# Kernel tuning notes

Hardware: AMD Instinct MI355X
Metric: run time of the kernel (lower is better)

Reference implementation:

```python
import jax, jax.numpy as jnp
import numpy as np

B, S, D_IN, D_OUT = 4, 2048, 1024, 1024

def setup_inputs() -> dict:
    key = jax.random.key(0)
    k1, k2, k3, k4 = jax.random.split(key, 4)
    sc = 0.02
    return {
        "x": jax.random.normal(k1, (B, S, D_IN), dtype=jnp.float32),
        "Wq": jax.random.normal(k2, (D_OUT, D_IN), dtype=jnp.float32) * sc,
        "Wk": jax.random.normal(k3, (D_OUT, D_IN), dtype=jnp.float32) * sc,
        "Wv": jax.random.normal(k4, (D_OUT, D_IN), dtype=jnp.float32) * sc,
    }

def reference(x, Wq, Wk, Wv):
    # torch Linear: y = x @ W.T  (weights stored [out, in])
    b, n, _ = x.shape
    q = jnp.einsum('bnd,od->bno', x, Wq)  # [B,S,D_OUT]
    k = jnp.einsum('bnd,od->bno', x, Wk)
    v = jnp.einsum('bnd,od->bno', x, Wv)
    scores = jnp.einsum('bqd,bkd->bqk', q, k)  # [B,S,S]
    # causal mask: positions j > i masked to -inf BEFORE scaling (matches source)
    causal = jnp.triu(jnp.ones((n, n), dtype=bool), k=1)
    scores = jnp.where(causal[None, :, :], -jnp.inf, scores)
    scale = 1.0 / jnp.sqrt(jnp.float32(k.shape[-1]))
    attn = jax.nn.softmax(scores * scale, axis=-1)
    # NOTE: source calls dropout but discards its output -> no-op
    return jnp.einsum('bqk,bkd->bqd', attn, v)
```

## Files before the change

kernel.cpp:

```cpp
#include <hip/hip_runtime.h>
#include <hip/hip_bf16.h>
#include <hip/hip_fp16.h>


using bf16 = __hip_bfloat16;
typedef __bf16 bf16x8 __attribute__((ext_vector_type(8)));
typedef float f32x4 __attribute__((ext_vector_type(4)));

__device__ __forceinline__ void load_lds_16B(const void* g, void* l) {
  __builtin_amdgcn_global_load_lds(
      (const __attribute__((address_space(1))) unsigned int*)g,
      (__attribute__((address_space(3))) unsigned int*)l, 16, 0, 0);
}

template <int N>
__device__ __forceinline__ void waitcnt_vm() {
  if constexpr (N == 6) asm volatile("s_waitcnt vmcnt(6)" ::: "memory");
  else if constexpr (N == 5) asm volatile("s_waitcnt vmcnt(5)" ::: "memory");
  else asm volatile("s_waitcnt vmcnt(0)" ::: "memory");
}

__device__ __forceinline__ int swz(int o) { return o ^ (((o >> 7) & 7) << 4); }

template <int M_REP, int OUT, bool CSKIP, bool KLIM>
__global__ __launch_bounds__(512, 2) void gemm8p(
    const bf16* __restrict__ A, const bf16* __restrict__ Bm, void* __restrict__ Cv,
    int K, int lda, int ldb, int ldc, long sAz, long sBz, long sCzBytes) {
  constexpr int BM = M_REP * 32, BN = 256;
  constexpr int MH2 = M_REP / 2;
  constexpr int AKC = BM * 64;
  constexpr int BKC = BN * 64;
  constexpr int DBSTR = 2 * AKC + 2 * BKC;
  constexpr int ACALLS = AKC / 8192;
  constexpr int VM_LEAVE = ACALLS + 4;

  const int tn = blockIdx.x, tm = blockIdx.y, z = blockIdx.z;
  if (CSKIP && tn > tm) return;
  A += (long)z * sAz;
  Bm += (long)z * sBz;
  char* C = (char*)Cv + (long)z * sCzBytes;

  int kEnd = K;
  if (KLIM) kEnd = min(tm * BM + BM, K);
  const int nt = kEnd >> 6;
  const int NI = nt >> 1;

  __shared__ __align__(128) char sm[2 * DBSTR];
  const int tid = threadIdx.x, lane = tid & 63, wv = tid >> 6;
  const int wr = wv >> 2, wc = wv & 3;
  const int ldsw = wv * 1024;

  const char* srcA[ACALLS];
  const char* srcB[2];
#pragma unroll
  for (int c = 0; c < ACALLS; c++) {
    int os = swz(c * 8192 + tid * 16);
    srcA[c] = (const char*)(A + ((long)tm * BM + (os >> 6)) * lda) + (os & 63);
  }
#pragma unroll
  for (int c = 0; c < 2; c++) {
    int os = swz(c * 8192 + tid * 16);
    srcB[c] = (const char*)(Bm + ((long)tn * BN + (os >> 6)) * ldb) + (os & 63);
  }
  auto stageA = [&](int t, int kc) {
#pragma unroll
    for (int c = 0; c < ACALLS; c++)
      load_lds_16B(srcA[c] + (long)t * 128 + kc * 64,
                   sm + (t & 1) * DBSTR + kc * AKC + c * 8192 + ldsw);
  };
  auto stageB = [&](int t, int kc) {
#pragma unroll
    for (int c = 0; c < 2; c++)
      load_lds_16B(srcB[c] + (long)t * 128 + kc * 64,
                   sm + (t & 1) * DBSTR + 2 * AKC + kc * BKC + c * 8192 + ldsw);
  };

  int aoff[M_REP], boff[4];
#pragma unroll
  for (int m = 0; m < M_REP; m++)
    aoff[m] = swz((wr * (M_REP * 16) + m * 16 + (lane & 15)) * 64 + (lane >> 4) * 16);
#pragma unroll
  for (int n = 0; n < 4; n++)
    boff[n] = 2 * AKC + swz((wc * 64 + n * 16 + (lane & 15)) * 64 + (lane >> 4) * 16);

  f32x4 acc[M_REP][4] = {};
  bf16x8 bfr[2][4];
  bf16x8 afrA[MH2], afrB[MH2];

#define LDB(DBUF, KC)                                                          \
  _Pragma("unroll") for (int n = 0; n < 4; n++)                                \
      bfr[KC][n] = *(const bf16x8*)(sm + (DBUF)*DBSTR + (KC)*BKC + boff[n]);
#define LDA(DBUF, KC, MH, DST)                                                 \
  _Pragma("unroll") for (int m = 0; m < MH2; m++)                              \
      DST[m] = *(const bf16x8*)(sm + (DBUF)*DBSTR + (KC)*AKC + aoff[(MH)*MH2 + m]);
#define MFMAS(KC, MH, AFR)                                                     \
  __builtin_amdgcn_s_setprio(1);                                               \
  _Pragma("unroll") for (int m = 0; m < MH2; m++)                              \
      _Pragma("unroll") for (int n = 0; n < 4; n++)                            \
          acc[(MH)*MH2 + m][n] = __builtin_amdgcn_mfma_f32_16x16x32_bf16(      \
              AFR[m], bfr[KC][n], acc[(MH)*MH2 + m][n], 0, 0, 0);              \
  __builtin_amdgcn_s_setprio(0);
#define BAR1()                                                                 \
  __builtin_amdgcn_s_barrier();                                                \
  asm volatile("s_waitcnt lgkmcnt(0)" ::: "memory");                           \
  __builtin_amdgcn_sched_barrier(0);
#define BAR2() __builtin_amdgcn_s_barrier();

  stageB(0, 0); stageA(0, 0); stageB(0, 1); stageA(0, 1);
  stageB(1, 0); stageA(1, 0); stageB(1, 1);
  waitcnt_vm<VM_LEAVE>();
  __builtin_amdgcn_s_barrier();

  for (int i = 0; i < NI - 1; i++) {
    const int ta = 2 * i, tb = 2 * i + 1;
    LDB(0, 0); LDA(0, 0, 0, afrA); stageA(tb, 1);     BAR1(); MFMAS(0, 0, afrA); BAR2();
    LDA(0, 0, 1, afrB);            stageB(ta + 2, 0); BAR1(); MFMAS(0, 1, afrB); BAR2();
    LDB(0, 1); LDA(0, 1, 0, afrA); stageA(ta + 2, 0); BAR1(); MFMAS(1, 0, afrA); BAR2();
    LDA(0, 1, 1, afrB);            stageB(ta + 2, 1);
    waitcnt_vm<VM_LEAVE>();                           BAR1(); MFMAS(1, 1, afrB); BAR2();
    LDB(1, 0); LDA(1, 0, 0, afrA); stageA(ta + 2, 1); BAR1(); MFMAS(0, 0, afrA); BAR2();
    LDA(1, 0, 1, afrB);            stageB(tb + 2, 0); BAR1(); MFMAS(0, 1, afrB); BAR2();
    LDB(1, 1); LDA(1, 1, 0, afrA); stageA(tb + 2, 0); BAR1(); MFMAS(1, 0, afrA); BAR2();
    LDA(1, 1, 1, afrB);            stageB(tb + 2, 1);
    waitcnt_vm<VM_LEAVE>();                           BAR1(); MFMAS(1, 1, afrB); BAR2();
  }
  {
    const int tb = nt - 1;
    LDB(0, 0); LDA(0, 0, 0, afrA); stageA(tb, 1); BAR1(); MFMAS(0, 0, afrA); BAR2();
    LDA(0, 0, 1, afrB);                           BAR1(); MFMAS(0, 1, afrB); BAR2();
    LDB(0, 1); LDA(0, 1, 0, afrA);                BAR1(); MFMAS(1, 0, afrA); BAR2();
    LDA(0, 1, 1, afrB); waitcnt_vm<0>();          BAR1(); MFMAS(1, 1, afrB); BAR2();
    LDB(1, 0); LDA(1, 0, 0, afrA);                BAR1(); MFMAS(0, 0, afrA); BAR2();
    LDA(1, 0, 1, afrB);                           BAR1(); MFMAS(0, 1, afrB); BAR2();
    LDB(1, 1); LDA(1, 1, 0, afrA);                BAR1(); MFMAS(1, 0, afrA); BAR2();
    LDA(1, 1, 1, afrB);                           BAR1(); MFMAS(1, 1, afrB); BAR2();
  }
#undef LDB
#undef LDA
#undef MFMAS
#undef BAR1
#undef BAR2

  const int cr0 = tm * BM + wr * (M_REP * 16) + (lane >> 4) * 4;
  const int cc0 = tn * BN + wc * 64 + (lane & 15);
#pragma unroll
  for (int m = 0; m < M_REP; m++)
#pragma unroll
    for (int n = 0; n < 4; n++)
#pragma unroll
      for (int j = 0; j < 4; j++) {
        long row = cr0 + m * 16 + j;
        long col = cc0 + n * 16;
        if (OUT == 1)
          ((bf16*)C)[row * (long)ldc + col] = __float2bfloat16(acc[m][n][j]);
        else if (OUT == 2)
          ((__half*)C)[row * (long)ldc + col] = __float2half(acc[m][n][j]);
        else
          ((float*)C)[row * (long)ldc + col] = acc[m][n][j];
      }
}

__global__ __launch_bounds__(256) void cvt_all(const float* __restrict__ x,
                                               const float* __restrict__ wq,
                                               const float* __restrict__ wk,
                                               const float* __restrict__ wv,
                                               bf16* __restrict__ xb,
                                               bf16* __restrict__ wb) {
  const int b = blockIdx.x;
  const float* src;
  bf16* dst;
  int i;
  if (b < 8192) { src = x; dst = xb; i = b * 256 + threadIdx.x; }
  else if (b < 9216) { src = wq; dst = wb; i = (b - 8192) * 256 + threadIdx.x; }
  else if (b < 10240) { src = wk; dst = wb + 1048576; i = (b - 9216) * 256 + threadIdx.x; }
  else { src = wv; dst = wb + 2097152; i = (b - 10240) * 256 + threadIdx.x; }
  float4 f = ((const float4*)src)[i];
  union { bf16 h[4]; uint2 u; } o;
  o.h[0] = __float2bfloat16(f.x);
  o.h[1] = __float2bfloat16(f.y);
  o.h[2] = __float2bfloat16(f.z);
  o.h[3] = __float2bfloat16(f.w);
  ((uint2*)dst)[i] = o.u;
}

typedef short short4v __attribute__((ext_vector_type(4)));

__global__ __launch_bounds__(256) void softmax_causal(const __half* __restrict__ Sc,
                                                      bf16* __restrict__ P) {
  const int i = blockIdx.x, b = blockIdx.y;
  const long base = ((long)b * 2048 + i) * 2048;
  const __half* row = Sc + base;
  bf16* prow = P + base;
  const int tid = threadIdx.x, lane = tid & 63, wv = tid >> 6;
  const int len = i + 1;

  float v[8];
  float m = -3.3e38f;
  {
    const int j0 = tid * 8;
    union { short4v s[2]; __half h[8]; } u;
    u.s[0] = *(const short4v*)(row + j0);
    u.s[1] = *(const short4v*)(row + j0 + 4);
#pragma unroll
    for (int e = 0; e < 8; e++) {
      float t = __half2float(u.h[e]);
      v[e] = (j0 + e < len) ? t : -3.3e38f;
      m = fmaxf(m, v[e]);
    }
  }
  for (int o = 32; o; o >>= 1) m = fmaxf(m, __shfl_xor(m, o));
  __shared__ float redm[4], reds[4];
  if (lane == 0) redm[wv] = m;
  __syncthreads();
  m = fmaxf(fmaxf(redm[0], redm[1]), fmaxf(redm[2], redm[3]));

  const float scale = 0.03125f;
  float e8[8];
  float s = 0.f;
  {
    const int j0 = tid * 8;
#pragma unroll
    for (int e = 0; e < 8; e++) {
      float t = (j0 + e < len) ? __expf((v[e] - m) * scale) : 0.f;
      e8[e] = t;
      s += t;
    }
  }
  for (int o = 32; o; o >>= 1) s += __shfl_xor(s, o);
  if (lane == 0) reds[wv] = s;
  __syncthreads();
  s = reds[0] + reds[1] + reds[2] + reds[3];
  const float inv = 1.0f / s;
  {
    const int j0 = tid * 8;
    union { bf16 h[8]; uint4 u4; } o;
#pragma unroll
    for (int e = 0; e < 8; e++) o.h[e] = __float2bfloat16(e8[e] * inv);
    *(uint4*)(prow + j0) = o.u4;
  }
}

__global__ __launch_bounds__(256) void transposeV(const bf16* __restrict__ V,
                                                  bf16* __restrict__ Vt) {
  __shared__ bf16 t[32][33];
  const int b = blockIdx.z;
  const int s0 = blockIdx.x << 5;
  const int d0 = blockIdx.y << 5;
  const bf16* Vb = V + (long)b * 2048 * 3072;
  bf16* Vtb = Vt + (long)b * 1024 * 2048;
  const int lx = threadIdx.x & 31, ly = threadIdx.x >> 5;
#pragma unroll
  for (int r = 0; r < 32; r += 8)
    t[r + ly][lx] = Vb[(long)(s0 + r + ly) * 3072 + d0 + lx];
  __syncthreads();
#pragma unroll
  for (int r = 0; r < 32; r += 8)
    Vtb[(long)(d0 + r + ly) * 2048 + s0 + lx] = t[lx][r + ly];
}

extern "C" void kernel_launch(void* const* d_in, const int* in_sizes, int n_in,
                              void* d_out, int out_size, void* d_ws, size_t ws_size,
                              hipStream_t stream) {
  const float* x = (const float*)d_in[0];
  const float* Wq = (const float*)d_in[1];
  const float* Wk = (const float*)d_in[2];
  const float* Wv = (const float*)d_in[3];

  const long MBy = 1 << 20;
  char* ws = (char*)d_ws;
  bf16* Cqkv = (bf16*)(ws);
  bf16* Vt = (bf16*)(ws + 48 * MBy);
  bf16* P = (bf16*)(ws + 64 * MBy);
  __half* Sc = (__half*)(ws + 96 * MBy);
  bf16* xb = (bf16*)(ws + 96 * MBy);
  bf16* Wb = (bf16*)(ws + 112 * MBy);

  cvt_all<<<11264, 256, 0, stream>>>(x, Wq, Wk, Wv, xb, Wb);

  gemm8p<4, 1, false, false><<<dim3(12, 64), 512, 0, stream>>>(
      xb, Wb, Cqkv, 1024, 1024, 1024, 3072, 0L, 0L, 0L);

  transposeV<<<dim3(64, 32, 4), 256, 0, stream>>>(Cqkv + 2048, Vt);

  gemm8p<8, 2, true, false><<<dim3(8, 8, 4), 512, 0, stream>>>(
      Cqkv, Cqkv + 1024, Sc, 1024, 3072, 3072, 2048,
      2048L * 3072, 2048L * 3072, 2048L * 2048 * 2);

  softmax_causal<<<dim3(2048, 4), 256, 0, stream>>>(Sc, P);

  gemm8p<4, 0, false, true><<<dim3(4, 16, 4), 512, 0, stream>>>(
      P, Vt, d_out, 2048, 2048, 2048, 1024,
      2048L * 2048, 1024L * 2048, 2048L * 1024 * 4);
}
```

Before: 169.4 us.

## Generalize GEMM kernel tiling and retune tiles per stage with reversed causal order

Replaces the fixed 512-thread GEMM template with one parameterized by block tile, warp grid, staging thread count and occupancy. Each of the three GEMMs (QKV projection, QK^T scores, PV) gets its own tile shape and warp count. Finer-grained causal block skipping on the score GEMM, plus reversed row order for the K-limited PV GEMM so the heaviest tiles launch first. This trades register and LDS pressure and occupancy for better load balance and reuse, and relies on the padded even tile count staying correct for the causal PV K-range.

```diff
diff --git a/kernel.cpp b/kernel.cpp
--- a/kernel.cpp
+++ b/kernel.cpp
@@ -15,80 +15,92 @@
 
 template <int N>
 __device__ __forceinline__ void waitcnt_vm() {
-  if constexpr (N == 6) asm volatile("s_waitcnt vmcnt(6)" ::: "memory");
+  if constexpr (N == 10) asm volatile("s_waitcnt vmcnt(10)" ::: "memory");
+  else if constexpr (N == 9) asm volatile("s_waitcnt vmcnt(9)" ::: "memory");
+  else if constexpr (N == 8) asm volatile("s_waitcnt vmcnt(8)" ::: "memory");
+  else if constexpr (N == 6) asm volatile("s_waitcnt vmcnt(6)" ::: "memory");
   else if constexpr (N == 5) asm volatile("s_waitcnt vmcnt(5)" ::: "memory");
   else asm volatile("s_waitcnt vmcnt(0)" ::: "memory");
 }
 
 __device__ __forceinline__ int swz(int o) { return o ^ (((o >> 7) & 7) << 4); }
 
-template <int M_REP, int OUT, bool CSKIP, bool KLIM>
-__global__ __launch_bounds__(512, 2) void gemm8p(
+template <int BM, int BN, int WM, int WN, int STHR, int OCC, int OUT,
+          bool CSKIP, bool KLIM>
+__global__ __launch_bounds__(WM* WN * 64, OCC) void gemmT(
     const bf16* __restrict__ A, const bf16* __restrict__ Bm, void* __restrict__ Cv,
     int K, int lda, int ldb, int ldc, long sAz, long sBz, long sCzBytes) {
-  constexpr int BM = M_REP * 32, BN = 256;
-  constexpr int MH2 = M_REP / 2;
+  constexpr int MR = BM / WM / 16, NR = BN / WN / 16, MH2 = MR / 2;
   constexpr int AKC = BM * 64;
   constexpr int BKC = BN * 64;
-  constexpr int DBSTR = 2 * AKC + 2 * BKC;
-  constexpr int ACALLS = AKC / 8192;
-  constexpr int VM_LEAVE = ACALLS + 4;
-
-  const int tn = blockIdx.x, tm = blockIdx.y, z = blockIdx.z;
-  if (CSKIP && tn > tm) return;
+  constexpr int DBSTR = 2 * (AKC + BKC);
+  constexpr int CHUNK = STHR * 16;
+  constexpr int ACALLS = AKC / CHUNK;
+  constexpr int BCALLS = BKC / CHUNK;
+  constexpr int VM_LEAVE = ACALLS + 2 * BCALLS;
+
+  const int tn = blockIdx.x, z = blockIdx.z;
+  const int tm = KLIM ? (gridDim.y - 1 - blockIdx.y) : blockIdx.y;
+  if (CSKIP && (long)tn * BN >= (long)tm * BM + BM) return;
   A += (long)z * sAz;
   Bm += (long)z * sBz;
   char* C = (char*)Cv + (long)z * sCzBytes;
 
   int kEnd = K;
   if (KLIM) kEnd = min(tm * BM + BM, K);
-  const int nt = kEnd >> 6;
+  int nt = kEnd >> 6;
+  if (KLIM) nt = (nt + 1) & ~1;
   const int NI = nt >> 1;
 
   __shared__ __align__(128) char sm[2 * DBSTR];
   const int tid = threadIdx.x, lane = tid & 63, wv = tid >> 6;
-  const int wr = wv >> 2, wc = wv & 3;
-  const int ldsw = wv * 1024;
-
+  const int wr = wv / WN, wc = wv % WN;
+  const int ldsw = (tid >> 6) * 1024;
+
+  const int ts = (tid < STHR) ? tid : 0;
   const char* srcA[ACALLS];
-  const char* srcB[2];
+  const char* srcB[BCALLS];
 #pragma unroll
   for (int c = 0; c < ACALLS; c++) {
-    int os = swz(c * 8192 + tid * 16);
+    int os = swz(c * CHUNK + ts * 16);
     srcA[c] = (const char*)(A + ((long)tm * BM + (os >> 6)) * lda) + (os & 63);
   }
 #pragma unroll
-  for (int c = 0; c < 2; c++) {
-    int os = swz(c * 8192 + tid * 16);
+  for (int c = 0; c < BCALLS; c++) {
+    int os = swz(c * CHUNK + ts * 16);
     srcB[c] = (const char*)(Bm + ((long)tn * BN + (os >> 6)) * ldb) + (os & 63);
   }
   auto stageA = [&](int t, int kc) {
-#pragma unroll
-    for (int c = 0; c < ACALLS; c++)
-      load_lds_16B(srcA[c] + (long)t * 128 + kc * 64,
-                   sm + (t & 1) * DBSTR + kc * AKC + c * 8192 + ldsw);
+    if (tid < STHR) {
+#pragma unroll
+      for (int c = 0; c < ACALLS; c++)
+        load_lds_16B(srcA[c] + (long)t * 128 + kc * 64,
+                     sm + (t & 1) * DBSTR + kc * AKC + c * CHUNK + ldsw);
+    }
   };
   auto stageB = [&](int t, int kc) {
-#pragma unroll
-    for (int c = 0; c < 2; c++)
-      load_lds_16B(srcB[c] + (long)t * 128 + kc * 64,
-                   sm + (t & 1) * DBSTR + 2 * AKC + kc * BKC + c * 8192 + ldsw);
+    if (tid < STHR) {
+#pragma unroll
+      for (int c = 0; c < BCALLS; c++)
+        load_lds_16B(srcB[c] + (long)t * 128 + kc * 64,
+                     sm + (t & 1) * DBSTR + 2 * AKC + kc * BKC + c * CHUNK + ldsw);
+    }
   };
 
-  int aoff[M_REP], boff[4];
-#pragma unroll
-  for (int m = 0; m < M_REP; m++)
-    aoff[m] = swz((wr * (M_REP * 16) + m * 16 + (lane & 15)) * 64 + (lane >> 4) * 16);
-#pragma unroll
-  for (int n = 0; n < 4; n++)
-    boff[n] = 2 * AKC + swz((wc * 64 + n * 16 + (lane & 15)) * 64 + (lane >> 4) * 16);
-
-  f32x4 acc[M_REP][4] = {};
-  bf16x8 bfr[2][4];
+  int aoff[MR], boff[NR];
+#pragma unroll
+  for (int m = 0; m < MR; m++)
+    aoff[m] = swz((wr * (BM / WM) + m * 16 + (lane & 15)) * 64 + (lane >> 4) * 16);
+#pragma unroll
+  for (int n = 0; n < NR; n++)
+    boff[n] = 2 * AKC + swz((wc * (BN / WN) + n * 16 + (lane & 15)) * 64 + (lane >> 4) * 16);
+
+  f32x4 acc[MR][NR] = {};
+  bf16x8 bfr[2][NR];
   bf16x8 afrA[MH2], afrB[MH2];
 
 #define LDB(DBUF, KC)                                                          \
-  _Pragma("unroll") for (int n = 0; n < 4; n++)                                \
+  _Pragma("unroll") for (int n = 0; n < NR; n++)                               \
       bfr[KC][n] = *(const bf16x8*)(sm + (DBUF)*DBSTR + (KC)*BKC + boff[n]);
 #define LDA(DBUF, KC, MH, DST)                                                 \
   _Pragma("unroll") for (int m = 0; m < MH2; m++)                              \
@@ -96,7 +108,7 @@
 #define MFMAS(KC, MH, AFR)                                                     \
   __builtin_amdgcn_s_setprio(1);                                               \
   _Pragma("unroll") for (int m = 0; m < MH2; m++)                              \
-      _Pragma("unroll") for (int n = 0; n < 4; n++)                            \
+      _Pragma("unroll") for (int n = 0; n < NR; n++)                           \
           acc[(MH)*MH2 + m][n] = __builtin_amdgcn_mfma_f32_16x16x32_bf16(      \
               AFR[m], bfr[KC][n], acc[(MH)*MH2 + m][n], 0, 0, 0);              \
   __builtin_amdgcn_s_setprio(0);
@@ -141,12 +153,12 @@
 #undef BAR1
 #undef BAR2
 
-  const int cr0 = tm * BM + wr * (M_REP * 16) + (lane >> 4) * 4;
-  const int cc0 = tn * BN + wc * 64 + (lane & 15);
-#pragma unroll
-  for (int m = 0; m < M_REP; m++)
-#pragma unroll
-    for (int n = 0; n < 4; n++)
+  const int cr0 = tm * BM + wr * (BM / WM) + (lane >> 4) * 4;
+  const int cc0 = tn * BN + wc * (BN / WN) + (lane & 15);
+#pragma unroll
+  for (int m = 0; m < MR; m++)
+#pragma unroll
+    for (int n = 0; n < NR; n++)
 #pragma unroll
       for (int j = 0; j < 4; j++) {
         long row = cr0 + m * 16 + j;
@@ -277,18 +289,18 @@
 
   cvt_all<<<11264, 256, 0, stream>>>(x, Wq, Wk, Wv, xb, Wb);
 
-  gemm8p<4, 1, false, false><<<dim3(12, 64), 512, 0, stream>>>(
+  gemmT<256, 192, 2, 3, 256, 1, 1, false, false><<<dim3(16, 32), 384, 0, stream>>>(
       xb, Wb, Cqkv, 1024, 1024, 1024, 3072, 0L, 0L, 0L);
 
   transposeV<<<dim3(64, 32, 4), 256, 0, stream>>>(Cqkv + 2048, Vt);
 
-  gemm8p<8, 2, true, false><<<dim3(8, 8, 4), 512, 0, stream>>>(
+  gemmT<256, 128, 2, 2, 256, 1, 2, true, false><<<dim3(16, 8, 4), 256, 0, stream>>>(
       Cqkv, Cqkv + 1024, Sc, 1024, 3072, 3072, 2048,
       2048L * 3072, 2048L * 3072, 2048L * 2048 * 2);
 
   softmax_causal<<<dim3(2048, 4), 256, 0, stream>>>(Sc, P);
 
-  gemm8p<4, 0, false, true><<<dim3(4, 16, 4), 512, 0, stream>>>(
+  gemmT<64, 256, 1, 4, 256, 2, 0, false, true><<<dim3(4, 32, 4), 256, 0, stream>>>(
       P, Vt, d_out, 2048, 2048, 2048, 1024,
       2048L * 2048, 1024L * 2048, 2048L * 1024 * 4);
 }
```

Result: slower. 189.3 us (+11.7%).
